# Kernel optimization log

Measured on AMD Instinct MI355X. Metric: run time of the kernel, lower is better.

## Reference

```python
import jax, jax.numpy as jnp
import numpy as np

N_CLASSES = 80
SEG_LEN = 512          # boxes per class (uniform segments)
H = 128                # hidden_size
DH = 2 * H             # decoder hidden (= concat of bidirectional encoder final hiddens)
EMB = 32               # decoder_input_dim
SOS, EOS = 2, 3


def _gru_cell(x, h, Wih, Whh, bih, bhh):
    # PyTorch GRU cell math. x:(in,), h:(hid,), Wih:(3*hid,in), Whh:(3*hid,hid)
    gi = Wih @ x + bih
    gh = Whh @ h + bhh
    i_r, i_z, i_n = jnp.split(gi, 3)
    h_r, h_z, h_n = jnp.split(gh, 3)
    r = jax.nn.sigmoid(i_r + h_r)
    z = jax.nn.sigmoid(i_z + h_z)
    n = jnp.tanh(i_n + r * h_n)
    return (1.0 - z) * n + z * h


def _gru_seq(xs, h0, Wih, Whh, bih, bhh):
    # xs: (T, in); returns final hidden (hid,) and all hiddens (T, hid)
    def step(h, x):
        h2 = _gru_cell(x, h, Wih, Whh, bih, bhh)
        return h2, h2
    hT, hs = jax.lax.scan(step, h0, xs)
    return hT, hs

# vmap over the 80 classes (per-class weights)
_run_gru = jax.vmap(_gru_seq, in_axes=(0, 0, 0, 0, 0, 0))


def setup_inputs() -> dict:
    key = jax.random.key(0)
    ks = jax.random.split(key, 32)
    N = N_CLASSES * SEG_LEN
    s = 0.05
    inp = {
        "feat": jax.random.normal(ks[0], (N, 1024), jnp.float32),
        "score": jax.random.uniform(ks[1], (N, 1), jnp.float32),
        "box": jax.random.uniform(ks[2], (N, 4), jnp.float32),
        "origin_score": jax.random.uniform(ks[3], (N, 91), jnp.float32),
        "labels": jax.random.randint(ks[4], (N,), 0, 2, jnp.int64),
        "weights": jax.random.uniform(ks[5], (N,), jnp.float32),
        "unique_class": jnp.ones((N_CLASSES,), jnp.int64),
        "unique_class_len": jnp.arange(N_CLASSES + 1, dtype=jnp.int64) * SEG_LEN,
        # shared linears
        "appear_W": jax.random.normal(ks[6], (H, 1024), jnp.float32) * s,
        "appear_b": jnp.zeros((H,), jnp.float32),
        "featlin_W": jax.random.normal(ks[7], (H, H + 96), jnp.float32) * s,
        "featlin_b": jnp.zeros((H,), jnp.float32),
        # per-class bidirectional encoder GRUs
        "enc_Wih_f": jax.random.normal(ks[8], (N_CLASSES, 3 * H, H), jnp.float32) * s,
        "enc_Whh_f": jax.random.normal(ks[9], (N_CLASSES, 3 * H, H), jnp.float32) * s,
        "enc_bih_f": jnp.zeros((N_CLASSES, 3 * H), jnp.float32),
        "enc_bhh_f": jnp.zeros((N_CLASSES, 3 * H), jnp.float32),
        "enc_Wih_b": jax.random.normal(ks[10], (N_CLASSES, 3 * H, H), jnp.float32) * s,
        "enc_Whh_b": jax.random.normal(ks[11], (N_CLASSES, 3 * H, H), jnp.float32) * s,
        "enc_bih_b": jnp.zeros((N_CLASSES, 3 * H), jnp.float32),
        "enc_bhh_b": jnp.zeros((N_CLASSES, 3 * H), jnp.float32),
        # decoder
        "dec_emb": jax.random.normal(ks[12], (4, EMB), jnp.float32) * s,
        "dec_Wih": jax.random.normal(ks[13], (N_CLASSES, 3 * DH, EMB), jnp.float32) * s,
        "dec_Whh": jax.random.normal(ks[14], (N_CLASSES, 3 * DH, DH), jnp.float32) * s,
        "dec_bih": jnp.zeros((N_CLASSES, 3 * DH), jnp.float32),
        "dec_bhh": jnp.zeros((N_CLASSES, 3 * DH), jnp.float32),
        "out_W": jax.random.normal(ks[15], (4, DH), jnp.float32) * s,
        "out_b": jnp.zeros((4,), jnp.float32),
    }
    return inp


def reference(feat, score, box, origin_score, labels, weights, unique_class,
              unique_class_len, appear_W, appear_b, featlin_W, featlin_b,
              enc_Wih_f, enc_Whh_f, enc_bih_f, enc_bhh_f,
              enc_Wih_b, enc_Whh_b, enc_bih_b, enc_bhh_b,
              dec_emb, dec_Wih, dec_Whh, dec_bih, dec_bhh, out_W, out_b):
    # --- shared feature encoding ---
    x = jax.nn.relu(feat @ appear_W.T + appear_b)                    # (N, H)
    allf = jnp.concatenate([x, score, box, origin_score], axis=1)    # (N, H+96)
    enc_feat = jax.nn.relu(allf @ featlin_W.T + featlin_b)           # (N, H)

    # --- per-class bidirectional encoder (uniform segments) ---
    seg = enc_feat.reshape(N_CLASSES, SEG_LEN, H)
    eos = jnp.ones((N_CLASSES, 1, H), enc_feat.dtype)                # encoder_EOS = ones
    enc_in = jnp.concatenate([seg, eos], axis=1)                     # (80, L+1, H)
    h0 = jnp.zeros((N_CLASSES, H), enc_feat.dtype)
    h_f, _ = _run_gru(enc_in, h0, enc_Wih_f, enc_Whh_f, enc_bih_f, enc_bhh_f)
    h_b, _ = _run_gru(enc_in[:, ::-1], h0, enc_Wih_b, enc_Whh_b, enc_bih_b, enc_bhh_b)
    dec_h0 = jnp.concatenate([h_f, h_b], axis=-1)                    # (80, 2H)

    # --- per-class decoder with teacher forcing (SOS then gold labels) ---
    emb = dec_emb[labels].reshape(N_CLASSES, SEG_LEN, EMB)
    sos = jnp.broadcast_to(dec_emb[SOS], (N_CLASSES, 1, EMB))
    dec_in = jnp.concatenate([sos, emb], axis=1)                     # (80, L+1, EMB)
    _, dec_hs = _run_gru(dec_in, dec_h0, dec_Wih, dec_Whh, dec_bih, dec_bhh)

    logits = dec_hs.reshape(-1, DH) @ out_W.T + out_b                # (80*(L+1), 4)
    output = jax.nn.log_softmax(logits, axis=-1)
    return output, labels, weights
```

## Files before the change

### kernel.cpp

```cpp
#include <hip/hip_runtime.h>


typedef __fp16 h2v __attribute__((ext_vector_type(2)));

__device__ __forceinline__ h2v pk2(float a, float b) {
  return __builtin_amdgcn_cvt_pkrtz(a, b);
}
__device__ __forceinline__ unsigned h2u(h2v h) { return __builtin_bit_cast(unsigned, h); }
__device__ __forceinline__ h2v u2h(unsigned u) { return __builtin_bit_cast(h2v, u); }
__device__ __forceinline__ float fdot2f(h2v a, h2v b, float c) {
  return __builtin_amdgcn_fdot2(a, b, c, false);
}
__device__ __forceinline__ float sigf(float x) { return 1.f / (1.f + __expf(-x)); }
__device__ __forceinline__ float tanhfast(float x) { return 2.f / (1.f + __expf(-2.f * x)) - 1.f; }

__device__ __forceinline__ uint4 pack8u(float4 a, float4 b) {
  uint4 o;
  o.x = h2u(pk2(a.x, a.y)); o.y = h2u(pk2(a.z, a.w));
  o.z = h2u(pk2(b.x, b.y)); o.w = h2u(pk2(b.z, b.w));
  return o;
}

__device__ __forceinline__ float dotu4(uint4 cv, h2v a0, h2v a1, h2v a2, h2v a3,
                                       float acc) {
  acc = fdot2f(u2h(cv.x), a0, acc);
  acc = fdot2f(u2h(cv.y), a1, acc);
  acc = fdot2f(u2h(cv.z), a2, acc);
  acc = fdot2f(u2h(cv.w), a3, acc);
  return acc;
}

template <int CTRL>
__device__ __forceinline__ float dppadd(float acc, float v) {
  int r = __builtin_amdgcn_update_dpp(0, __float_as_int(v), CTRL, 0xF, 0xF, true);
  return acc + __int_as_float(r);
}
__device__ __forceinline__ float swz4add(float acc, float v) {
  return acc + __int_as_float(__builtin_amdgcn_ds_swizzle(__float_as_int(v), 0x101F));
}

__device__ __forceinline__ float reduce8s(float p0, float p1, float p2, float p3,
                                          float p4, float p5, float p6, float p7) {
  p0 = dppadd<0xB1>(p0, p1);
  p2 = dppadd<0xB1>(p2, p3);
  p4 = dppadd<0xB1>(p4, p5);
  p6 = dppadd<0xB1>(p6, p7);
  p0 = dppadd<0x4E>(p0, p2);
  p4 = dppadd<0x4E>(p4, p6);
  p0 = swz4add(p0, p4);
  p0 = dppadd<0x128>(p0, p0);
  return p0;
}

#define BAR_LGKM()                                     \
  asm volatile("s_waitcnt lgkmcnt(0)" ::: "memory");   \
  __builtin_amdgcn_s_barrier();                        \
  asm volatile("" ::: "memory");

__global__ void k_fill_misc(const float* __restrict__ score, const float* __restrict__ box,
                            const float* __restrict__ orig, float* __restrict__ allf) {
  int i = blockIdx.x * blockDim.x + threadIdx.x;
  if (i >= 40960 * 96) return;
  int row = i / 96, k = i - row * 96;
  float v;
  if (k == 0) v = score[row];
  else if (k < 5) v = box[row * 4 + (k - 1)];
  else v = orig[(size_t)row * 91 + (k - 5)];
  allf[(size_t)row * 224 + 128 + k] = v;
}

__global__ __launch_bounds__(256) void k_gemm_appear(
    const float* __restrict__ A, const float* __restrict__ W,
    const float* __restrict__ bias, float* __restrict__ allf) {
  __shared__ float As[32][68];
  __shared__ float Ws[32][132];
  const int tid = threadIdx.x;
  const int tx = tid & 15, ty = tid >> 4;
  const int r0 = blockIdx.x * 64;
  const int lr = tid >> 3;
  const int lk = (tid & 7) * 4;
  float acc[4][8];
#pragma unroll
  for (int i = 0; i < 4; ++i)
#pragma unroll
    for (int j = 0; j < 8; ++j) acc[i][j] = 0.f;

  for (int k0 = 0; k0 < 1024; k0 += 32) {
#pragma unroll
    for (int i = 0; i < 2; ++i) {
      int rr = lr + i * 32;
      float4 v = *(const float4*)(A + (size_t)(r0 + rr) * 1024 + k0 + lk);
      As[lk + 0][rr] = v.x; As[lk + 1][rr] = v.y; As[lk + 2][rr] = v.z; As[lk + 3][rr] = v.w;
    }
#pragma unroll
    for (int i = 0; i < 4; ++i) {
      int wr = lr + i * 32;
      float4 v = *(const float4*)(W + (size_t)wr * 1024 + k0 + lk);
      Ws[lk + 0][wr] = v.x; Ws[lk + 1][wr] = v.y; Ws[lk + 2][wr] = v.z; Ws[lk + 3][wr] = v.w;
    }
    __syncthreads();
#pragma unroll
    for (int kk = 0; kk < 32; ++kk) {
      float4 a = *(const float4*)&As[kk][ty * 4];
      float4 w0 = *(const float4*)&Ws[kk][tx * 8];
      float4 w1 = *(const float4*)&Ws[kk][tx * 8 + 4];
      float av[4] = {a.x, a.y, a.z, a.w};
      float wv[8] = {w0.x, w0.y, w0.z, w0.w, w1.x, w1.y, w1.z, w1.w};
#pragma unroll
      for (int i = 0; i < 4; ++i)
#pragma unroll
        for (int j = 0; j < 8; ++j) acc[i][j] = fmaf(av[i], wv[j], acc[i][j]);
    }
    __syncthreads();
  }
#pragma unroll
  for (int i = 0; i < 4; ++i) {
    int row = r0 + ty * 4 + i;
#pragma unroll
    for (int j = 0; j < 8; ++j) {
      int col = tx * 8 + j;
      float v = acc[i][j] + bias[col];
      allf[(size_t)row * 224 + col] = fmaxf(v, 0.f);
    }
  }
}

__global__ __launch_bounds__(256) void k_gemm_featlin(
    const float* __restrict__ A, const float* __restrict__ W,
    const float* __restrict__ bias, unsigned* __restrict__ encf2) {
  __shared__ float As[32][68];
  __shared__ float Ws[32][132];
  const int tid = threadIdx.x;
  const int tx = tid & 15, ty = tid >> 4;
  const int r0 = blockIdx.x * 64;
  const int lr = tid >> 3;
  const int lk = (tid & 7) * 4;
  float acc[4][8];
#pragma unroll
  for (int i = 0; i < 4; ++i)
#pragma unroll
    for (int j = 0; j < 8; ++j) acc[i][j] = 0.f;

  for (int k0 = 0; k0 < 224; k0 += 32) {
#pragma unroll
    for (int i = 0; i < 2; ++i) {
      int rr = lr + i * 32;
      float4 v = *(const float4*)(A + (size_t)(r0 + rr) * 224 + k0 + lk);
      As[lk + 0][rr] = v.x; As[lk + 1][rr] = v.y; As[lk + 2][rr] = v.z; As[lk + 3][rr] = v.w;
    }
#pragma unroll
    for (int i = 0; i < 4; ++i) {
      int wr = lr + i * 32;
      float4 v = *(const float4*)(W + (size_t)wr * 224 + k0 + lk);
      Ws[lk + 0][wr] = v.x; Ws[lk + 1][wr] = v.y; Ws[lk + 2][wr] = v.z; Ws[lk + 3][wr] = v.w;
    }
    __syncthreads();
#pragma unroll
    for (int kk = 0; kk < 32; ++kk) {
      float4 a = *(const float4*)&As[kk][ty * 4];
      float4 w0 = *(const float4*)&Ws[kk][tx * 8];
      float4 w1 = *(const float4*)&Ws[kk][tx * 8 + 4];
      float av[4] = {a.x, a.y, a.z, a.w};
      float wv[8] = {w0.x, w0.y, w0.z, w0.w, w1.x, w1.y, w1.z, w1.w};
#pragma unroll
      for (int i = 0; i < 4; ++i)
#pragma unroll
        for (int j = 0; j < 8; ++j) acc[i][j] = fmaf(av[i], wv[j], acc[i][j]);
    }
    __syncthreads();
  }
#pragma unroll
  for (int i = 0; i < 4; ++i) {
    int row = r0 + ty * 4 + i;
    unsigned* orow = encf2 + (size_t)row * 64;
#pragma unroll
    for (int p = 0; p < 4; ++p) {
      int col = tx * 8 + 2 * p;
      float a = fmaxf(acc[i][2 * p] + bias[col], 0.f);
      float b = fmaxf(acc[i][2 * p + 1] + bias[col + 1], 0.f);
      orow[tx * 4 + p] = h2u(pk2(a, b));
    }
  }
}

__global__ __launch_bounds__(256) void k_dec_gi(
    const float* __restrict__ Wih, const float* __restrict__ bih,
    const float* __restrict__ emb, float* __restrict__ gi) {
  __shared__ float e[4][32];
  const int c = blockIdx.x, tid = threadIdx.x;
  if (tid < 128) e[tid >> 5][tid & 31] = emb[tid];
  __syncthreads();
#pragma unroll
  for (int i = 0; i < 3; ++i) {
    int r = tid + i * 256;
    const float* w = Wih + ((size_t)c * 768 + r) * 32;
    float b = bih[(size_t)c * 768 + r];
    float a0 = b, a1 = b, a2 = b, a3 = b;
#pragma unroll
    for (int k = 0; k < 32; ++k) {
      float wv = w[k];
      a0 = fmaf(wv, e[0][k], a0);
      a1 = fmaf(wv, e[1][k], a1);
      a2 = fmaf(wv, e[2][k], a2);
      a3 = fmaf(wv, e[3][k], a3);
    }
    gi[((size_t)c * 4 + 0) * 768 + r] = a0;
    gi[((size_t)c * 4 + 1) * 768 + r] = a1;
    gi[((size_t)c * 4 + 2) * 768 + r] = a2;
    gi[((size_t)c * 4 + 3) * 768 + r] = a3;
  }
}

__global__ __launch_bounds__(512) void k_pack_dec(
    const float* __restrict__ Whh, uint4* __restrict__ wpk) {
  const int c = blockIdx.x / 48, ic = blockIdx.x % 48;
  const int tid = threadIdx.x;
  const int G = tid >> 4, m = tid & 15, mw = m & 7;
  const int gt = ic >> 4, k = (ic & 15) >> 1, hf = ic & 1;
  const int row = gt * 256 + 8 * G + (k ^ mw);
  const float* src = Whh + ((size_t)c * 768 + row) * 256 + 16 * m + 8 * hf;
  wpk[((size_t)c * 48 + ic) * 512 + tid] =
      pack8u(*(const float4*)src, *(const float4*)(src + 4));
}

#define ELOAD(gt, k, DST)                                                          \
  {                                                                                \
    int rid_ = (k) ^ mw;                                                           \
    const float* Mx_ = ((k) & 1) ? baseB : baseA;                                  \
    const float4* ps_ =                                                            \
        (const float4*)(Mx_ + ((size_t)((gt) * 128 + 4 * G + (rid_ >> 1))) * 128 + \
                        8 * m);                                                    \
    DST = pack8u(ps_[0], ps_[1]);                                                  \
  }                                                                                \
  __builtin_amdgcn_sched_barrier(0);

__global__ __launch_bounds__(512) void k_enc_gru(
    const unsigned* __restrict__ encf2,
    const float* __restrict__ WihF, const float* __restrict__ WhhF,
    const float* __restrict__ bihF, const float* __restrict__ bhhF,
    const float* __restrict__ WihB, const float* __restrict__ WhhB,
    const float* __restrict__ bihB, const float* __restrict__ bhhB,
    float* __restrict__ dec_h0) {
  const int blk = blockIdx.x;
  const int c = blk >> 1, dir = blk & 1;
  const int tid = threadIdx.x;
  const int G = tid >> 4, m = tid & 15, mw = m & 7;

  const float* Wih = (dir ? WihB : WihF) + (size_t)c * 384 * 128;
  const float* Whh = (dir ? WhhB : WhhF) + (size_t)c * 384 * 128;
  const float* bih = (dir ? bihB : bihF) + (size_t)c * 384;
  const float* bhh = (dir ? bhhB : bhhF) + (size_t)c * 384;

  const float* baseA = (mw & 1) ? Whh : Wih;
  const float* baseB = (mw & 1) ? Wih : Whh;

  __shared__ __align__(16) unsigned x2s[2][64];
  __shared__ __align__(16) unsigned h2s[2][64];
  __shared__ __align__(16) uint4 wle[8 * 512];

  uint4 er0, er1, er2, er3, er4, er5, er6, er7;
  uint4 ez0, ez1, ez2, ez3, ez4, ez5, ez6, ez7;
  ELOAD(0, 0, er0) ELOAD(0, 1, er1) ELOAD(0, 2, er2) ELOAD(0, 3, er3)
  ELOAD(0, 4, er4) ELOAD(0, 5, er5) ELOAD(0, 6, er6) ELOAD(0, 7, er7)
  ELOAD(1, 0, ez0) ELOAD(1, 1, ez1) ELOAD(1, 2, ez2) ELOAD(1, 3, ez3)
  ELOAD(1, 4, ez4) ELOAD(1, 5, ez5) ELOAD(1, 6, ez6) ELOAD(1, 7, ez7)
  {
    uint4 t0;
    ELOAD(2, 0, t0) wle[0 * 512 + tid] = t0;
    ELOAD(2, 1, t0) wle[1 * 512 + tid] = t0;
    ELOAD(2, 2, t0) wle[2 * 512 + tid] = t0;
    ELOAD(2, 3, t0) wle[3 * 512 + tid] = t0;
    ELOAD(2, 4, t0) wle[4 * 512 + tid] = t0;
    ELOAD(2, 5, t0) wle[5 * 512 + tid] = t0;
    ELOAD(2, 6, t0) wle[6 * 512 + tid] = t0;
    ELOAD(2, 7, t0) wle[7 * 512 + tid] = t0;
  }

  const int u = 4 * G + (mw >> 1);
  const float brz_r = bih[u] + bhh[u];
  const float brz_z = bih[128 + u] + bhh[128 + u];
  const float b_in = bih[256 + u];
  const float b_hn = bhh[256 + u];

  if (tid < 64) h2s[0][tid] = 0u;
  if (tid >= 448) {
    int lane = tid - 448;
    x2s[0][lane] = (dir == 0) ? encf2[((size_t)c * 512 + 0) * 64 + lane] : 0x3C003C00u;
  }
  float hreg = 0.f;
  __syncthreads();

  const uint4* wl = wle + tid;

  for (int t = 0; t <= 512; ++t) {
    unsigned xpre = 0;
    if (tid >= 448 && t < 512) {
      int tn = t + 1, lane = tid - 448;
      int row = (dir == 0) ? ((tn < 512) ? tn : -1) : (512 - tn);
      xpre = (row < 0) ? 0x3C003C00u : encf2[((size_t)c * 512 + row) * 64 + lane];
    }
    uint4 xv = ((const uint4*)&x2s[t & 1][0])[m];
    uint4 hv = ((const uint4*)&h2s[t & 1][0])[m];
    h2v x0 = u2h(xv.x), x1 = u2h(xv.y), x2 = u2h(xv.z), x3 = u2h(xv.w);
    h2v hh0 = u2h(hv.x), hh1 = u2h(hv.y), hh2 = u2h(hv.z), hh3 = u2h(hv.w);
    bool oddl = (mw & 1);
    h2v a0 = oddl ? hh0 : x0, a1 = oddl ? hh1 : x1, a2 = oddl ? hh2 : x2, a3 = oddl ? hh3 : x3;
    h2v b0 = oddl ? x0 : hh0, b1 = oddl ? x1 : hh1, b2 = oddl ? x2 : hh2, b3 = oddl ? x3 : hh3;
#define EA(ch) dotu4(ch, a0, a1, a2, a3, 0.f)
#define EB(ch) dotu4(ch, b0, b1, b2, b3, 0.f)
    float vR = reduce8s(EA(er0), EB(er1), EA(er2), EB(er3),
                        EA(er4), EB(er5), EA(er6), EB(er7));
    float vZ = reduce8s(EA(ez0), EB(ez1), EA(ez2), EB(ez3),
                        EA(ez4), EB(ez5), EA(ez6), EB(ez7));
    float vN = reduce8s(EA(wl[0 * 512]), EB(wl[1 * 512]), EA(wl[2 * 512]), EB(wl[3 * 512]),
                        EA(wl[4 * 512]), EB(wl[5 * 512]), EA(wl[6 * 512]), EB(wl[7 * 512]));
#undef EA
#undef EB
    float oR = __shfl_xor(vR, 1, 64);
    float oZ = __shfl_xor(vZ, 1, 64);
    float oN = __shfl_xor(vN, 1, 64);
    float r = sigf(vR + oR + brz_r);
    float z = sigf(vZ + oZ + brz_z);
    float i_n = oddl ? oN : vN;
    float h_n = oddl ? vN : oN;
    float n = tanhfast(i_n + b_in + r * (h_n + b_hn));
    float hn = (1.f - z) * n + z * hreg;
    hreg = hn;
    float prt = __shfl_xor(hn, 2, 64);
    if (m < 8 && (mw & 3) == 0) h2s[(t + 1) & 1][2 * G + (mw >> 2)] = h2u(pk2(hn, prt));
    if (tid >= 448 && t < 512) x2s[(t + 1) & 1][tid - 448] = xpre;
    BAR_LGKM();
  }
  if ((m < 8) && ((mw & 1) == 0))
    dec_h0[(size_t)c * 256 + dir * 128 + u] = hreg;
}

#define CONSX(sa, sb) dotu4(sb, g4, g5, g6, g7, dotu4(sa, g0, g1, g2, g3, 0.f))

__global__ __launch_bounds__(512) void k_dec_gru(
    const uint4* __restrict__ wpk, const float* __restrict__ bhh,
    const float* __restrict__ gi, const float* __restrict__ h0,
    const int* __restrict__ labels, unsigned* __restrict__ dhs2) {
  const int c = blockIdx.x, tid = threadIdx.x;
  const int G = tid >> 4, m = tid & 15, mw = m & 7;

  __shared__ __align__(16) unsigned h2s[2][128];
  __shared__ int labs[513];
  __shared__ __align__(16) uint4 wlds[18 * 512];

  const uint4* wp = wpk + (size_t)c * 48 * 512 + tid;

  for (int j = 0; j < 18; ++j) wlds[j * 512 + tid] = wp[(12 + j) * 512];
  __builtin_amdgcn_sched_barrier(0);
  uint4 ra0 = wp[0 * 512], ra1 = wp[1 * 512], ra2 = wp[2 * 512], ra3 = wp[3 * 512];
  uint4 ra4 = wp[4 * 512], ra5 = wp[5 * 512], ra6 = wp[6 * 512], ra7 = wp[7 * 512];
  __builtin_amdgcn_sched_barrier(0);
  uint4 ra8 = wp[8 * 512], ra9 = wp[9 * 512], ra10 = wp[10 * 512], ra11 = wp[11 * 512];
  __builtin_amdgcn_sched_barrier(0);

  const int u = 8 * G + mw;
  const float bb0 = bhh[(size_t)c * 768 + u];
  const float bb1 = bhh[(size_t)c * 768 + 256 + u];
  const float bb2 = bhh[(size_t)c * 768 + 512 + u];
  const float* gib = gi + (size_t)c * 4 * 768;
  unsigned* dout = dhs2 + (size_t)c * 513 * 128 + 4 * G + (mw >> 1);

  if (tid < 512) labs[tid + 1] = labels[(size_t)c * 512 + tid];
  if (tid == 0) labs[0] = 2;
  float hreg = h0[(size_t)c * 256 + u];
  {
    float oth = __shfl_xor(hreg, 1, 64);
    if (m < 8 && (mw & 1) == 0) h2s[0][4 * G + (mw >> 1)] = h2u(pk2(hreg, oth));
  }
  __syncthreads();

  const uint4* wl = wlds + tid;

  for (int t = 0; t <= 512; ++t) {
    uint4 sa0 = wp[30 * 512], sa1 = wp[31 * 512], sa2 = wp[32 * 512], sa3 = wp[33 * 512];
    uint4 sa4 = wp[34 * 512], sa5 = wp[35 * 512], sa6 = wp[36 * 512], sa7 = wp[37 * 512];
    uint4 ha = ((const uint4*)&h2s[t & 1][0])[2 * m];
    uint4 hb = ((const uint4*)&h2s[t & 1][0])[2 * m + 1];
    h2v g0 = u2h(ha.x), g1 = u2h(ha.y), g2 = u2h(ha.z), g3 = u2h(ha.w);
    h2v g4 = u2h(hb.x), g5 = u2h(hb.y), g6 = u2h(hb.z), g7 = u2h(hb.w);
    int sel = labs[t];
    const float* gp = gib + sel * 768;
    float giR = gp[u], giZ = gp[256 + u], giN = gp[512 + u];
    float p0 = CONSX(ra0, ra1), p1 = CONSX(ra2, ra3);
    float p2 = CONSX(ra4, ra5), p3 = CONSX(ra6, ra7);
    float p4 = CONSX(ra8, ra9), p5 = CONSX(ra10, ra11);
    float p6 = CONSX(wl[0 * 512], wl[1 * 512]);
    float p7 = CONSX(wl[2 * 512], wl[3 * 512]);
    float rsum = reduce8s(p0, p1, p2, p3, p4, p5, p6, p7);
    uint4 sb0 = wp[38 * 512], sb1 = wp[39 * 512], sb2 = wp[40 * 512], sb3 = wp[41 * 512];
    uint4 sb4 = wp[42 * 512], sb5 = wp[43 * 512], sb6 = wp[44 * 512], sb7 = wp[45 * 512];
    uint4 sb8 = wp[46 * 512], sb9 = wp[47 * 512];
    p0 = CONSX(wl[4 * 512], wl[5 * 512]);
    p1 = CONSX(wl[6 * 512], wl[7 * 512]);
    p2 = CONSX(wl[8 * 512], wl[9 * 512]);
    p3 = CONSX(wl[10 * 512], wl[11 * 512]);
    p4 = CONSX(wl[12 * 512], wl[13 * 512]);
    p5 = CONSX(wl[14 * 512], wl[15 * 512]);
    p6 = CONSX(wl[16 * 512], wl[17 * 512]);
    p7 = CONSX(sa0, sa1);
    float zsum = reduce8s(p0, p1, p2, p3, p4, p5, p6, p7);
    p0 = CONSX(sa2, sa3);
    p1 = CONSX(sa4, sa5);
    p2 = CONSX(sa6, sa7);
    p3 = CONSX(sb0, sb1);
    p4 = CONSX(sb2, sb3);
    p5 = CONSX(sb4, sb5);
    p6 = CONSX(sb6, sb7);
    p7 = CONSX(sb8, sb9);
    float nsum = reduce8s(p0, p1, p2, p3, p4, p5, p6, p7);
    float r = sigf(giR + rsum + bb0);
    float z = sigf(giZ + zsum + bb1);
    float n = tanhfast(giN + r * (nsum + bb2));
    float hn = (1.f - z) * n + z * hreg;
    hreg = hn;
    float oth = __shfl_xor(hn, 1, 64);
    if (m < 8 && (mw & 1) == 0) {
      unsigned pk = h2u(pk2(hn, oth));
      h2s[(t + 1) & 1][4 * G + (mw >> 1)] = pk;
      dout[(size_t)t * 128] = pk;
    }
    BAR_LGKM();
  }
}

__global__ __launch_bounds__(256) void k_out(
    const unsigned* __restrict__ dhs2, const float* __restrict__ outW,
    const float* __restrict__ outB, float* __restrict__ out) {
  int row = blockIdx.x * 4 + (threadIdx.x >> 6);
  if (row >= 41040) return;
  int lane = threadIdx.x & 63;
  const unsigned* hp = dhs2 + (size_t)row * 128 + 2 * lane;
  h2v ha = u2h(hp[0]), hb = u2h(hp[1]);
  float h0f = (float)ha[0], h1f = (float)ha[1], h2f = (float)hb[0], h3f = (float)hb[1];
  float p0, p1, p2, p3;
  {
    const float* w0 = outW + 4 * lane;
    const float* w1 = outW + 256 + 4 * lane;
    const float* w2 = outW + 512 + 4 * lane;
    const float* w3 = outW + 768 + 4 * lane;
    p0 = h0f * w0[0] + h1f * w0[1] + h2f * w0[2] + h3f * w0[3];
    p1 = h0f * w1[0] + h1f * w1[1] + h2f * w1[2] + h3f * w1[3];
    p2 = h0f * w2[0] + h1f * w2[1] + h2f * w2[2] + h3f * w2[3];
    p3 = h0f * w3[0] + h1f * w3[1] + h2f * w3[2] + h3f * w3[3];
  }
#pragma unroll
  for (int off = 32; off > 0; off >>= 1) {
    p0 += __shfl_xor(p0, off, 64);
    p1 += __shfl_xor(p1, off, 64);
    p2 += __shfl_xor(p2, off, 64);
    p3 += __shfl_xor(p3, off, 64);
  }
  if (lane == 0) {
    float l0 = p0 + outB[0], l1 = p1 + outB[1], l2 = p2 + outB[2], l3 = p3 + outB[3];
    float mm = fmaxf(fmaxf(l0, l1), fmaxf(l2, l3));
    float s = __expf(l0 - mm) + __expf(l1 - mm) + __expf(l2 - mm) + __expf(l3 - mm);
    float lse = mm + __logf(s);
    float* o = out + (size_t)row * 4;
    o[0] = l0 - lse; o[1] = l1 - lse; o[2] = l2 - lse; o[3] = l3 - lse;
  }
}

__global__ void k_passthrough(const int* __restrict__ labels,
                              const float* __restrict__ weights,
                              float* __restrict__ out) {
  int i = blockIdx.x * blockDim.x + threadIdx.x;
  if (i < 40960) {
    out[164160 + i] = (float)labels[i];
    out[164160 + 40960 + i] = weights[i];
  }
}

extern "C" void kernel_launch(void* const* d_in, const int* in_sizes, int n_in,
                              void* d_out, int out_size, void* d_ws, size_t ws_size,
                              hipStream_t stream) {
  (void)in_sizes; (void)n_in; (void)out_size; (void)ws_size;
  const float* feat = (const float*)d_in[0];
  const float* score = (const float*)d_in[1];
  const float* box = (const float*)d_in[2];
  const float* orig = (const float*)d_in[3];
  const int* labels = (const int*)d_in[4];
  const float* weights = (const float*)d_in[5];
  const float* appear_W = (const float*)d_in[8];
  const float* appear_b = (const float*)d_in[9];
  const float* featlin_W = (const float*)d_in[10];
  const float* featlin_b = (const float*)d_in[11];
  const float* eWihF = (const float*)d_in[12];
  const float* eWhhF = (const float*)d_in[13];
  const float* ebihF = (const float*)d_in[14];
  const float* ebhhF = (const float*)d_in[15];
  const float* eWihB = (const float*)d_in[16];
  const float* eWhhB = (const float*)d_in[17];
  const float* ebihB = (const float*)d_in[18];
  const float* ebhhB = (const float*)d_in[19];
  const float* dec_emb = (const float*)d_in[20];
  const float* dWih = (const float*)d_in[21];
  const float* dWhh = (const float*)d_in[22];
  const float* dbih = (const float*)d_in[23];
  const float* dbhh = (const float*)d_in[24];
  const float* outW = (const float*)d_in[25];
  const float* outB = (const float*)d_in[26];
  float* out = (float*)d_out;

  char* ws = (char*)d_ws;
  float* allf = (float*)ws;
  unsigned* encf2 = (unsigned*)(ws + (size_t)40960 * 224 * 4);
  float* dec_h0 = (float*)(ws + (size_t)40960 * 224 * 4 + (size_t)40960 * 64 * 4);
  float* dec_gi = dec_h0 + 80 * 256;
  unsigned* dhs2 = (unsigned*)(dec_gi + 80 * 4 * 768);
  uint4* wpack = (uint4*)allf;

  k_fill_misc<<<15360, 256, 0, stream>>>(score, box, orig, allf);
  k_gemm_appear<<<640, 256, 0, stream>>>(feat, appear_W, appear_b, allf);
  k_gemm_featlin<<<640, 256, 0, stream>>>(allf, featlin_W, featlin_b, encf2);
  k_pack_dec<<<80 * 48, 512, 0, stream>>>(dWhh, wpack);
  k_dec_gi<<<80, 256, 0, stream>>>(dWih, dbih, dec_emb, dec_gi);
  k_enc_gru<<<160, 512, 0, stream>>>(encf2, eWihF, eWhhF, ebihF, ebhhF,
                                     eWihB, eWhhB, ebihB, ebhhB, dec_h0);
  k_dec_gru<<<80, 512, 0, stream>>>(wpack, dbhh, dec_gi, dec_h0, labels, dhs2);
  k_out<<<10260, 256, 0, stream>>>(dhs2, outW, outB, out);
  k_passthrough<<<160, 256, 0, stream>>>(labels, weights, out);
}
```

Measured before the change: 1.552 ms.

## Widen encoder GRU to 1024 threads with all weights in registers

The encoder GRU kernel now launches 1024 threads per block instead of 512. Each thread holds a half-width slice of the r, z and n weight rows in registers, so the n-gate weights no longer need to be read from LDS on every step. The per-step dot products get shorter, and the reduction gains an extra cross-lane shuffle stage. In exchange, block-wide barriers now span twice as many waves and the register budget is pinned by a waves-per-EU attribute.

```diff
diff --git a/kernel.cpp b/kernel.cpp
--- a/kernel.cpp
+++ b/kernel.cpp
@@ -28,6 +28,10 @@
   acc = fdot2f(u2h(cv.z), a2, acc);
   acc = fdot2f(u2h(cv.w), a3, acc);
   return acc;
+}
+
+__device__ __forceinline__ float d2(uint2 w, uint2 a) {
+  return fdot2f(u2h(w.x), u2h(a.x), fdot2f(u2h(w.y), u2h(a.y), 0.f));
 }
 
 template <int CTRL>
@@ -223,18 +227,20 @@
       pack8u(*(const float4*)src, *(const float4*)(src + 4));
 }
 
-#define ELOAD(gt, k, DST)                                                          \
+#define E2LD(g, k, DST)                                                            \
   {                                                                                \
     int rid_ = (k) ^ mw;                                                           \
-    const float* Mx_ = ((k) & 1) ? baseB : baseA;                                  \
-    const float4* ps_ =                                                            \
-        (const float4*)(Mx_ + ((size_t)((gt) * 128 + 4 * G + (rid_ >> 1))) * 128 + \
-                        8 * m);                                                    \
-    DST = pack8u(ps_[0], ps_[1]);                                                  \
+    int ul_ = (rid_ >> 2) & 1, hf_ = rid_ & 1;                                     \
+    const float* Mx_ = ((rid_ >> 1) & 1) ? Whh : Wih;                              \
+    float4 v_ = *(const float4*)(Mx_ + ((size_t)((g) * 128 + 2 * G + ul_)) * 128 + \
+                                 hf_ * 64 + 4 * m);                                \
+    DST.x = h2u(pk2(v_.x, v_.y));                                                  \
+    DST.y = h2u(pk2(v_.z, v_.w));                                                  \
   }                                                                                \
   __builtin_amdgcn_sched_barrier(0);
 
-__global__ __launch_bounds__(512) void k_enc_gru(
+__global__ __launch_bounds__(1024)
+__attribute__((amdgpu_waves_per_eu(4, 4))) void k_enc_gru(
     const unsigned* __restrict__ encf2,
     const float* __restrict__ WihF, const float* __restrict__ WhhF,
     const float* __restrict__ bihF, const float* __restrict__ bhhF,
@@ -251,87 +257,73 @@
   const float* bih = (dir ? bihB : bihF) + (size_t)c * 384;
   const float* bhh = (dir ? bhhB : bhhF) + (size_t)c * 384;
 
-  const float* baseA = (mw & 1) ? Whh : Wih;
-  const float* baseB = (mw & 1) ? Wih : Whh;
-
   __shared__ __align__(16) unsigned x2s[2][64];
   __shared__ __align__(16) unsigned h2s[2][64];
-  __shared__ __align__(16) uint4 wle[8 * 512];
-
-  uint4 er0, er1, er2, er3, er4, er5, er6, er7;
-  uint4 ez0, ez1, ez2, ez3, ez4, ez5, ez6, ez7;
-  ELOAD(0, 0, er0) ELOAD(0, 1, er1) ELOAD(0, 2, er2) ELOAD(0, 3, er3)
-  ELOAD(0, 4, er4) ELOAD(0, 5, er5) ELOAD(0, 6, er6) ELOAD(0, 7, er7)
-  ELOAD(1, 0, ez0) ELOAD(1, 1, ez1) ELOAD(1, 2, ez2) ELOAD(1, 3, ez3)
-  ELOAD(1, 4, ez4) ELOAD(1, 5, ez5) ELOAD(1, 6, ez6) ELOAD(1, 7, ez7)
-  {
-    uint4 t0;
-    ELOAD(2, 0, t0) wle[0 * 512 + tid] = t0;
-    ELOAD(2, 1, t0) wle[1 * 512 + tid] = t0;
-    ELOAD(2, 2, t0) wle[2 * 512 + tid] = t0;
-    ELOAD(2, 3, t0) wle[3 * 512 + tid] = t0;
-    ELOAD(2, 4, t0) wle[4 * 512 + tid] = t0;
-    ELOAD(2, 5, t0) wle[5 * 512 + tid] = t0;
-    ELOAD(2, 6, t0) wle[6 * 512 + tid] = t0;
-    ELOAD(2, 7, t0) wle[7 * 512 + tid] = t0;
-  }
-
-  const int u = 4 * G + (mw >> 1);
+
+  uint2 wr0, wr1, wr2, wr3, wr4, wr5, wr6, wr7;
+  uint2 wz0, wz1, wz2, wz3, wz4, wz5, wz6, wz7;
+  uint2 wn0, wn1, wn2, wn3, wn4, wn5, wn6, wn7;
+  E2LD(0, 0, wr0) E2LD(0, 1, wr1) E2LD(0, 2, wr2) E2LD(0, 3, wr3)
+  E2LD(0, 4, wr4) E2LD(0, 5, wr5) E2LD(0, 6, wr6) E2LD(0, 7, wr7)
+  E2LD(1, 0, wz0) E2LD(1, 1, wz1) E2LD(1, 2, wz2) E2LD(1, 3, wz3)
+  E2LD(1, 4, wz4) E2LD(1, 5, wz5) E2LD(1, 6, wz6) E2LD(1, 7, wz7)
+  E2LD(2, 0, wn0) E2LD(2, 1, wn1) E2LD(2, 2, wn2) E2LD(2, 3, wn3)
+  E2LD(2, 4, wn4) E2LD(2, 5, wn5) E2LD(2, 6, wn6) E2LD(2, 7, wn7)
+
+  const int u = 2 * G + ((m >> 2) & 1);
   const float brz_r = bih[u] + bhh[u];
   const float brz_z = bih[128 + u] + bhh[128 + u];
   const float b_in = bih[256 + u];
   const float b_hn = bhh[256 + u];
 
   if (tid < 64) h2s[0][tid] = 0u;
-  if (tid >= 448) {
-    int lane = tid - 448;
+  if (tid >= 960) {
+    int lane = tid - 960;
     x2s[0][lane] = (dir == 0) ? encf2[((size_t)c * 512 + 0) * 64 + lane] : 0x3C003C00u;
   }
   float hreg = 0.f;
   __syncthreads();
 
-  const uint4* wl = wle + tid;
+  const bool s0 = (mw & 1), s1 = ((mw >> 1) & 1);
 
   for (int t = 0; t <= 512; ++t) {
     unsigned xpre = 0;
-    if (tid >= 448 && t < 512) {
-      int tn = t + 1, lane = tid - 448;
+    if (tid >= 960 && t < 512) {
+      int tn = t + 1, lane = tid - 960;
       int row = (dir == 0) ? ((tn < 512) ? tn : -1) : (512 - tn);
       xpre = (row < 0) ? 0x3C003C00u : encf2[((size_t)c * 512 + row) * 64 + lane];
     }
-    uint4 xv = ((const uint4*)&x2s[t & 1][0])[m];
-    uint4 hv = ((const uint4*)&h2s[t & 1][0])[m];
-    h2v x0 = u2h(xv.x), x1 = u2h(xv.y), x2 = u2h(xv.z), x3 = u2h(xv.w);
-    h2v hh0 = u2h(hv.x), hh1 = u2h(hv.y), hh2 = u2h(hv.z), hh3 = u2h(hv.w);
-    bool oddl = (mw & 1);
-    h2v a0 = oddl ? hh0 : x0, a1 = oddl ? hh1 : x1, a2 = oddl ? hh2 : x2, a3 = oddl ? hh3 : x3;
-    h2v b0 = oddl ? x0 : hh0, b1 = oddl ? x1 : hh1, b2 = oddl ? x2 : hh2, b3 = oddl ? x3 : hh3;
-#define EA(ch) dotu4(ch, a0, a1, a2, a3, 0.f)
-#define EB(ch) dotu4(ch, b0, b1, b2, b3, 0.f)
-    float vR = reduce8s(EA(er0), EB(er1), EA(er2), EB(er3),
-                        EA(er4), EB(er5), EA(er6), EB(er7));
-    float vZ = reduce8s(EA(ez0), EB(ez1), EA(ez2), EB(ez3),
-                        EA(ez4), EB(ez5), EA(ez6), EB(ez7));
-    float vN = reduce8s(EA(wl[0 * 512]), EB(wl[1 * 512]), EA(wl[2 * 512]), EB(wl[3 * 512]),
-                        EA(wl[4 * 512]), EB(wl[5 * 512]), EA(wl[6 * 512]), EB(wl[7 * 512]));
-#undef EA
-#undef EB
-    float oR = __shfl_xor(vR, 1, 64);
-    float oZ = __shfl_xor(vZ, 1, 64);
-    float oN = __shfl_xor(vN, 1, 64);
-    float r = sigf(vR + oR + brz_r);
-    float z = sigf(vZ + oZ + brz_z);
-    float i_n = oddl ? oN : vN;
-    float h_n = oddl ? vN : oN;
-    float n = tanhfast(i_n + b_in + r * (h_n + b_hn));
+    uint2 xl = *(const uint2*)&x2s[t & 1][2 * m];
+    uint2 xh = *(const uint2*)&x2s[t & 1][32 + 2 * m];
+    uint2 hl = *(const uint2*)&h2s[t & 1][2 * m];
+    uint2 hh = *(const uint2*)&h2s[t & 1][32 + 2 * m];
+    uint2 P0 = s1 ? (s0 ? hh : hl) : (s0 ? xh : xl);
+    uint2 P1 = s1 ? (s0 ? hl : hh) : (s0 ? xl : xh);
+    uint2 P2 = s1 ? (s0 ? xh : xl) : (s0 ? hh : hl);
+    uint2 P3 = s1 ? (s0 ? xl : xh) : (s0 ? hl : hh);
+    float vR = reduce8s(d2(wr0, P0), d2(wr1, P1), d2(wr2, P2), d2(wr3, P3),
+                        d2(wr4, P0), d2(wr5, P1), d2(wr6, P2), d2(wr7, P3));
+    float vZ = reduce8s(d2(wz0, P0), d2(wz1, P1), d2(wz2, P2), d2(wz3, P3),
+                        d2(wz4, P0), d2(wz5, P1), d2(wz6, P2), d2(wz7, P3));
+    float vN = reduce8s(d2(wn0, P0), d2(wn1, P1), d2(wn2, P2), d2(wn3, P3),
+                        d2(wn4, P0), d2(wn5, P1), d2(wn6, P2), d2(wn7, P3));
+    float vRh = vR + __shfl_xor(vR, 1, 64);
+    float vZh = vZ + __shfl_xor(vZ, 1, 64);
+    float vNh = vN + __shfl_xor(vN, 1, 64);
+    float vRc = vRh + __shfl_xor(vRh, 2, 64);
+    float vZc = vZh + __shfl_xor(vZh, 2, 64);
+    float nOth = __shfl_xor(vNh, 2, 64);
+    float r = sigf(vRc + brz_r);
+    float z = sigf(vZc + brz_z);
+    float n = tanhfast(vNh + b_in + r * (nOth + b_hn));
     float hn = (1.f - z) * n + z * hreg;
     hreg = hn;
-    float prt = __shfl_xor(hn, 2, 64);
-    if (m < 8 && (mw & 3) == 0) h2s[(t + 1) & 1][2 * G + (mw >> 2)] = h2u(pk2(hn, prt));
-    if (tid >= 448 && t < 512) x2s[(t + 1) & 1][tid - 448] = xpre;
+    float hnP = __shfl_xor(hn, 4, 64);
+    if (m == 0) h2s[(t + 1) & 1][G] = h2u(pk2(hn, hnP));
+    if (tid >= 960 && t < 512) x2s[(t + 1) & 1][tid - 960] = xpre;
     BAR_LGKM();
   }
-  if ((m < 8) && ((mw & 1) == 0))
+  if (((m & 3) == 0) && (m < 8))
     dec_h0[(size_t)c * 256 + dir * 128 + u] = hreg;
 }
 
@@ -519,8 +511,8 @@
   k_gemm_featlin<<<640, 256, 0, stream>>>(allf, featlin_W, featlin_b, encf2);
   k_pack_dec<<<80 * 48, 512, 0, stream>>>(dWhh, wpack);
   k_dec_gi<<<80, 256, 0, stream>>>(dWih, dbih, dec_emb, dec_gi);
-  k_enc_gru<<<160, 512, 0, stream>>>(encf2, eWihF, eWhhF, ebihF, ebhhF,
-                                     eWihB, eWhhB, ebihB, ebhhB, dec_h0);
+  k_enc_gru<<<160, 1024, 0, stream>>>(encf2, eWihF, eWhhF, ebihF, ebhhF,
+                                      eWihB, eWhhB, ebihB, ebhhB, dec_h0);
   k_dec_gru<<<80, 512, 0, stream>>>(wpack, dbhh, dec_gi, dec_h0, labels, dhs2);
   k_out<<<10260, 256, 0, stream>>>(dhs2, outW, outB, out);
   k_passthrough<<<160, 256, 0, stream>>>(labels, weights, out);
```

Result: slower. 1.709 ms (+10.1%).
